# Kernel optimization log

Measured on AMD Instinct MI355X. Metric: run time of the kernel, lower is better.

## Reference

```python
import jax, jax.numpy as jnp
import numpy as np

VOCAB = 28996
EMBED = 512
N = 8192


def setup_inputs() -> dict:
    key = jax.random.key(0)
    k1, k2, k3, k4 = jax.random.split(key, 4)
    x = jax.random.normal(k1, (N, EMBED), dtype=jnp.float32)
    y = jax.random.randint(k2, (N,), 0, VOCAB, dtype=jnp.int64 if jax.config.jax_enable_x64 else jnp.int32)
    # nn.Linear params: weight (vocab, embed), bias (vocab,)
    W = jax.random.normal(k3, (VOCAB, EMBED), dtype=jnp.float32) * 0.02
    b = jax.random.normal(k4, (VOCAB,), dtype=jnp.float32) * 0.02
    return {"x": x, "y": y, "W": W, "b": b}


def reference(x, y, W, b):
    # Decoder: linear -> softmax over vocab (dim=1)
    logits = jnp.einsum("ne,ve->nv", x, W) + b          # (N, VOCAB)
    probs = jax.nn.softmax(logits, axis=1)              # first softmax (faithful to original)
    # nn.CrossEntropyLoss applied to probs: mean over nodes of
    #   logsumexp(probs) - probs[y]   (i.e., -log_softmax(probs)[y])
    logp = jax.nn.log_softmax(probs, axis=1)            # second (redundant) softmax pass
    nll = -jnp.take_along_axis(logp, y[:, None].astype(jnp.int32), axis=1)[:, 0]
    return jnp.mean(nll)
```

## Files before the change

### kernel.cpp

```cpp
#include <hip/hip_runtime.h>
#include <stdint.h>

#define VOCAB 28996
#define EMBED 512
#define NROWS 8192
#define VPAD  29056
#define LOG2E 1.4426950408889634f
#define WSCALE 16.0f
#define INV_WSCALE_L2E (LOG2E / 16.0f)

typedef __attribute__((ext_vector_type(4)))  int   i32x4;
typedef __attribute__((ext_vector_type(8)))  int   i32x8;
typedef __attribute__((ext_vector_type(16))) float f32x16;

__device__ __forceinline__ void gload_lds16(const void* g, void* l) {
  __builtin_amdgcn_global_load_lds(
      (__attribute__((address_space(1))) const void*)g,
      (__attribute__((address_space(3))) void*)l, 16, 0, 0);
}

__device__ __forceinline__ int pk_fp8x4(float a, float b, float c, float d) {
  int r = __builtin_amdgcn_cvt_pk_fp8_f32(a, b, 0, false);
  r = __builtin_amdgcn_cvt_pk_fp8_f32(c, d, r, true);
  return r;
}

__global__ void __launch_bounds__(256)
prep_kernel(const float* __restrict__ x, const float* __restrict__ W,
            const float* __restrict__ b, const int* __restrict__ y,
            int* __restrict__ xb, int* __restrict__ wb,
            float* __restrict__ py, float* __restrict__ sg) {
  const int bid = blockIdx.x;
  if (bid < 7264) {
    int i = (bid * 256 + threadIdx.x) * 8;
    const int VK = VOCAB * EMBED;
    int2 o;
    if (i < VK) {
      float4 v0 = *(const float4*)(W + i);
      float4 v1 = *(const float4*)(W + i + 4);
      o.x = pk_fp8x4(v0.x * WSCALE, v0.y * WSCALE, v0.z * WSCALE, v0.w * WSCALE);
      o.y = pk_fp8x4(v1.x * WSCALE, v1.y * WSCALE, v1.z * WSCALE, v1.w * WSCALE);
    } else { o.x = 0; o.y = 0; }
    *(int2*)(wb + i / 4) = o;
  } else if (bid < 9312) {
    int i = ((bid - 7264) * 256 + threadIdx.x) * 8;
    float4 v0 = *(const float4*)(x + i);
    float4 v1 = *(const float4*)(x + i + 4);
    int2 o;
    o.x = pk_fp8x4(v0.x, v0.y, v0.z, v0.w);
    o.y = pk_fp8x4(v1.x, v1.y, v1.z, v1.w);
    *(int2*)(xb + i / 4) = o;
  } else if (bid < 11360) {
    const int row  = ((bid - 9312) * 256 + threadIdx.x) >> 6;
    const int lane = threadIdx.x & 63;
    const int yr = y[row];
    const float4* xr = (const float4*)(x + (size_t)row * EMBED);
    const float4* wr = (const float4*)(W + (size_t)yr * EMBED);
    float d = 0.f;
#pragma unroll
    for (int t = 0; t < 2; ++t) {
      float4 a = xr[lane * 2 + t], c = wr[lane * 2 + t];
      d += a.x * c.x + a.y * c.y + a.z * c.z + a.w * c.w;
    }
#pragma unroll
    for (int m = 1; m < 64; m <<= 1) d += __shfl_xor(d, m);
    if (lane == 0) py[row] = __expf(d + b[yr]);
  } else {
    int i = (bid - 11360) * 256 + threadIdx.x;
    sg[i] = 0.f;
  }
}

__global__ void __launch_bounds__(512, 2)
gemm_stats_kernel(const uint8_t* __restrict__ xb, const uint8_t* __restrict__ wb,
                  const float* __restrict__ bias, float* __restrict__ sg) {
  __shared__ uint8_t lA[2][256 * 128];
  __shared__ uint8_t lB[2][256 * 128];

  const int tid  = threadIdx.x;
  const int lane = tid & 63;
  const int w    = tid >> 6;
  const int l31  = lane & 31;
  const int h    = lane >> 5;
  const int kx   = lane & 7;
  const int wr   = (w >> 2) * 128;
  const int wc   = (w & 3) * 64;
  const int rowBase = blockIdx.x * 256;
  const int colBase = blockIdx.y * 256;

  const int srow = lane >> 3;
  const int skel = (kx ^ srow) * 16;

  f32x16 acc[4][2];
#pragma unroll
  for (int i = 0; i < 4; ++i)
#pragma unroll
    for (int j = 0; j < 2; ++j)
#pragma unroll
      for (int r = 0; r < 16; ++r) acc[i][j][r] = 0.f;

  auto stage = [&](int buf, int k0) {
#pragma unroll
    for (int t = 0; t < 4; ++t) {
      const int c = w * 4 + t;
      const int ar = rowBase + c * 8;
      int br = colBase + c * 8;
      if (br > VPAD - 8) br = VPAD - 8;
      gload_lds16(xb + (size_t)(ar + srow) * EMBED + k0 + skel, &lA[buf][c * 1024]);
      gload_lds16(wb + (size_t)(br + srow) * EMBED + k0 + skel, &lB[buf][c * 1024]);
    }
  };

  stage(0, 0);

  const int aBase = (wr + l31) * 128;
  const int bBase = (wc + l31) * 128;

#pragma unroll
  for (int kt = 0; kt < 4; ++kt) {
    const int cur = kt & 1;
    __syncthreads();
    if (kt < 3) stage(cur ^ 1, (kt + 1) * 128);
    i32x8 bq[2][2];
#pragma unroll
    for (int kk = 0; kk < 2; ++kk) {
      const int c0 = ((kk * 4 + h * 2) ^ kx) << 4;
      const int c1 = c0 ^ 16;
#pragma unroll
      for (int ni = 0; ni < 2; ++ni) {
        const uint8_t* bp = &lB[cur][bBase + ni * 32 * 128];
        i32x4 lo = *(const i32x4*)(bp + c0);
        i32x4 hi = *(const i32x4*)(bp + c1);
        bq[kk][ni] = __builtin_shufflevector(lo, hi, 0, 1, 2, 3, 4, 5, 6, 7);
      }
    }
#pragma unroll
    for (int mi = 0; mi < 4; ++mi) {
      i32x8 af[2];
#pragma unroll
      for (int kk = 0; kk < 2; ++kk) {
        const int c0 = ((kk * 4 + h * 2) ^ kx) << 4;
        const int c1 = c0 ^ 16;
        const uint8_t* ap = &lA[cur][aBase + mi * 32 * 128];
        i32x4 lo = *(const i32x4*)(ap + c0);
        i32x4 hi = *(const i32x4*)(ap + c1);
        af[kk] = __builtin_shufflevector(lo, hi, 0, 1, 2, 3, 4, 5, 6, 7);
      }
      __builtin_amdgcn_s_setprio(1);
#pragma unroll
      for (int kk = 0; kk < 2; ++kk)
#pragma unroll
        for (int ni = 0; ni < 2; ++ni)
          acc[mi][ni] = __builtin_amdgcn_mfma_scale_f32_32x32x64_f8f6f4(
              af[kk], bq[kk][ni], acc[mi][ni], 0, 0, 0, 0x7F7F7F7F, 0, 0x7F7F7F7F);
      __builtin_amdgcn_s_setprio(0);
    }
  }

  float bvl[2];
#pragma unroll
  for (int ni = 0; ni < 2; ++ni) {
    const int col = colBase + wc + ni * 32 + l31;
    bvl[ni] = (col < VOCAB) ? bias[col] * LOG2E : -1e30f;
  }

#pragma unroll
  for (int p = 0; p < 2; ++p) {
    float sp[32];
#pragma unroll
    for (int q = 0; q < 2; ++q)
#pragma unroll
      for (int r = 0; r < 16; ++r)
        sp[q * 16 + r] =
            exp2f(fmaf(acc[p * 2 + q][0][r], INV_WSCALE_L2E, bvl[0])) +
            exp2f(fmaf(acc[p * 2 + q][1][r], INV_WSCALE_L2E, bvl[1]));

    float t1[16];
#pragma unroll
    for (int u = 0; u < 16; ++u) {
      float a = sp[2 * u]     + __shfl_xor(sp[2 * u],     1);
      float b = sp[2 * u + 1] + __shfl_xor(sp[2 * u + 1], 1);
      t1[u] = (l31 & 1) ? b : a;
    }
    float t2[8];
#pragma unroll
    for (int u = 0; u < 8; ++u) {
      float a = t1[2 * u]     + __shfl_xor(t1[2 * u],     2);
      float b = t1[2 * u + 1] + __shfl_xor(t1[2 * u + 1], 2);
      t2[u] = (l31 & 2) ? b : a;
    }
    float t3[4];
#pragma unroll
    for (int u = 0; u < 4; ++u) {
      float a = t2[2 * u]     + __shfl_xor(t2[2 * u],     4);
      float b = t2[2 * u + 1] + __shfl_xor(t2[2 * u + 1], 4);
      t3[u] = (l31 & 4) ? b : a;
    }
    float t4[2];
#pragma unroll
    for (int u = 0; u < 2; ++u) {
      float a = t3[2 * u]     + __shfl_xor(t3[2 * u],     8);
      float b = t3[2 * u + 1] + __shfl_xor(t3[2 * u + 1], 8);
      t4[u] = (l31 & 8) ? b : a;
    }
    {
      float a = t4[0] + __shfl_xor(t4[0], 16);
      float b = t4[1] + __shfl_xor(t4[1], 16);
      float ssum = (l31 & 16) ? b : a;
      const int v = l31;
      const int row = rowBase + wr + p * 64 + (v >> 4) * 32 +
                      (v & 3) + 8 * ((v & 15) >> 2) + 4 * h;
      atomicAdd(&sg[row], ssum);
    }
  }
}

__global__ void finalize_kernel(const float* __restrict__ sg, const float* __restrict__ py,
                                float* __restrict__ out) {
  __shared__ float red[256];
  float a = 0.f;
  for (int i = threadIdx.x; i < NROWS; i += 256)
    a += py[i] / sg[i];
  red[threadIdx.x] = a;
  __syncthreads();
  for (int st = 128; st > 0; st >>= 1) {
    if (threadIdx.x < st) red[threadIdx.x] += red[threadIdx.x + st];
    __syncthreads();
  }
  if (threadIdx.x == 0)
    out[0] = logf((float)(VOCAB + 1)) - red[0] * (1.f / (float)NROWS);
}

extern "C" void kernel_launch(void* const* d_in, const int* in_sizes, int n_in,
                              void* d_out, int out_size, void* d_ws, size_t ws_size,
                              hipStream_t stream) {
  const float* x = (const float*)d_in[0];
  const int*   y = (const int*)d_in[1];
  const float* W = (const float*)d_in[2];
  const float* b = (const float*)d_in[3];

  char* ws = (char*)d_ws;
  uint8_t* xb = (uint8_t*)ws;
  uint8_t* wb = (uint8_t*)(ws + 4194304);
  float*   sg = (float*)(ws + 4194304 + 14876672);
  float*   py = sg + NROWS;

  prep_kernel<<<11392, 256, 0, stream>>>(x, W, b, y, (int*)xb, (int*)wb, py, sg);
  gemm_stats_kernel<<<dim3(32, 114), 512, 0, stream>>>(xb, wb, b, sg);
  finalize_kernel<<<1, 256, 0, stream>>>(sg, py, (float*)d_out);
}
```

Before: 314.2 us.

## Interleave next-tile global-to-LDS loads with MFMA stages using explicit barriers

Restructures the K-loop of the FP8 GEMM so that prefetching of the next K tile is split across the mi iterations (A loads at mi=0, B loads at mi=1). The __syncthreads is replaced with explicit vmcnt/lgkmcnt waits, s_barrier and sched_barrier calls. The goal is to spread global memory issue between MFMA groups and keep waves in lockstep for better overlap. In exchange it adds more barriers per K step, which may cost sync overhead with only 4 K iterations.

```diff
diff --git a/kernel.cpp b/kernel.cpp
--- a/kernel.cpp
+++ b/kernel.cpp
@@ -99,19 +99,15 @@
 #pragma unroll
       for (int r = 0; r < 16; ++r) acc[i][j][r] = 0.f;
 
-  auto stage = [&](int buf, int k0) {
-#pragma unroll
-    for (int t = 0; t < 4; ++t) {
-      const int c = w * 4 + t;
-      const int ar = rowBase + c * 8;
-      int br = colBase + c * 8;
-      if (br > VPAD - 8) br = VPAD - 8;
-      gload_lds16(xb + (size_t)(ar + srow) * EMBED + k0 + skel, &lA[buf][c * 1024]);
-      gload_lds16(wb + (size_t)(br + srow) * EMBED + k0 + skel, &lB[buf][c * 1024]);
-    }
-  };
-
-  stage(0, 0);
+#pragma unroll
+  for (int t = 0; t < 4; ++t) {
+    const int c = w * 4 + t;
+    const int ar = rowBase + c * 8;
+    int br = colBase + c * 8;
+    if (br > VPAD - 8) br = VPAD - 8;
+    gload_lds16(xb + (size_t)(ar + srow) * EMBED + skel, &lA[0][c * 1024]);
+    gload_lds16(wb + (size_t)(br + srow) * EMBED + skel, &lB[0][c * 1024]);
+  }
 
   const int aBase = (wr + l31) * 128;
   const int bBase = (wc + l31) * 128;
@@ -119,33 +115,61 @@
 #pragma unroll
   for (int kt = 0; kt < 4; ++kt) {
     const int cur = kt & 1;
-    __syncthreads();
-    if (kt < 3) stage(cur ^ 1, (kt + 1) * 128);
+    asm volatile("s_waitcnt vmcnt(0)" ::: "memory");
+    __builtin_amdgcn_sched_barrier(0);
+    __builtin_amdgcn_s_barrier();
+
+    const uint8_t* __restrict__ Ab = lA[cur];
+    const uint8_t* __restrict__ Bb = lB[cur];
+    uint8_t* __restrict__ An = lA[cur ^ 1];
+    uint8_t* __restrict__ Bn = lB[cur ^ 1];
+    const int k1 = (kt + 1) * 128;
+
     i32x8 bq[2][2];
 #pragma unroll
-    for (int kk = 0; kk < 2; ++kk) {
-      const int c0 = ((kk * 4 + h * 2) ^ kx) << 4;
-      const int c1 = c0 ^ 16;
-#pragma unroll
-      for (int ni = 0; ni < 2; ++ni) {
-        const uint8_t* bp = &lB[cur][bBase + ni * 32 * 128];
-        i32x4 lo = *(const i32x4*)(bp + c0);
-        i32x4 hi = *(const i32x4*)(bp + c1);
-        bq[kk][ni] = __builtin_shufflevector(lo, hi, 0, 1, 2, 3, 4, 5, 6, 7);
+    for (int mi = 0; mi < 4; ++mi) {
+      if (mi == 0) {
+#pragma unroll
+        for (int kk = 0; kk < 2; ++kk) {
+          const int c0 = ((kk * 4 + h * 2) ^ kx) << 4;
+          const int c1 = c0 ^ 16;
+#pragma unroll
+          for (int ni = 0; ni < 2; ++ni) {
+            const uint8_t* bp = Bb + bBase + ni * 32 * 128;
+            i32x4 lo = *(const i32x4*)(bp + c0);
+            i32x4 hi = *(const i32x4*)(bp + c1);
+            bq[kk][ni] = __builtin_shufflevector(lo, hi, 0, 1, 2, 3, 4, 5, 6, 7);
+          }
+        }
       }
-    }
-#pragma unroll
-    for (int mi = 0; mi < 4; ++mi) {
       i32x8 af[2];
 #pragma unroll
       for (int kk = 0; kk < 2; ++kk) {
         const int c0 = ((kk * 4 + h * 2) ^ kx) << 4;
         const int c1 = c0 ^ 16;
-        const uint8_t* ap = &lA[cur][aBase + mi * 32 * 128];
+        const uint8_t* ap = Ab + aBase + mi * 32 * 128;
         i32x4 lo = *(const i32x4*)(ap + c0);
         i32x4 hi = *(const i32x4*)(ap + c1);
         af[kk] = __builtin_shufflevector(lo, hi, 0, 1, 2, 3, 4, 5, 6, 7);
       }
+      if (kt < 3 && mi < 2) {
+#pragma unroll
+        for (int t = 0; t < 4; ++t) {
+          const int c = w * 4 + t;
+          if (mi == 0) {
+            gload_lds16(xb + (size_t)(rowBase + c * 8 + srow) * EMBED + k1 + skel,
+                        An + c * 1024);
+          } else {
+            int br = colBase + c * 8;
+            if (br > VPAD - 8) br = VPAD - 8;
+            gload_lds16(wb + (size_t)(br + srow) * EMBED + k1 + skel,
+                        Bn + c * 1024);
+          }
+        }
+      }
+      __builtin_amdgcn_s_barrier();
+      asm volatile("s_waitcnt lgkmcnt(0)" ::: "memory");
+      __builtin_amdgcn_sched_barrier(0);
       __builtin_amdgcn_s_setprio(1);
 #pragma unroll
       for (int kk = 0; kk < 2; ++kk)
@@ -154,6 +178,7 @@
           acc[mi][ni] = __builtin_amdgcn_mfma_scale_f32_32x32x64_f8f6f4(
               af[kk], bq[kk][ni], acc[mi][ni], 0, 0, 0, 0x7F7F7F7F, 0, 0x7F7F7F7F);
       __builtin_amdgcn_s_setprio(0);
+      if (mi < 3) __builtin_amdgcn_s_barrier();
     }
   }
 
```

Result: slower. 324.7 us (+3.3%).

## Shrink GEMM tile to 128x256 with 256 threads and single-buffered LDS

Applied to the files above, without the earlier changes.

Changes the fused GEMM+softmax-stats kernel from 256x256 tiles with 8 waves and double-buffered LDS to 128x256 tiles with 4 waves and a single LDS buffer. Each k-step now loads, syncs, computes, and syncs again, with no prefetch overlap. The intent is to cut LDS use to 48KB per block so three blocks fit per CU, and to double the grid for better occupancy and load balance. In exchange it loses the software pipelining and the setprio hints, and each W tile is read twice as often.

```diff
diff --git a/kernel.cpp b/kernel.cpp
--- a/kernel.cpp
+++ b/kernel.cpp
@@ -71,11 +71,11 @@
   }
 }
 
-__global__ void __launch_bounds__(512, 2)
+__global__ void __launch_bounds__(256, 3)
 gemm_stats_kernel(const uint8_t* __restrict__ xb, const uint8_t* __restrict__ wb,
                   const float* __restrict__ bias, float* __restrict__ sg) {
-  __shared__ uint8_t lA[2][256 * 128];
-  __shared__ uint8_t lB[2][256 * 128];
+  __shared__ uint8_t lA[128 * 128];
+  __shared__ uint8_t lB[256 * 128];
 
   const int tid  = threadIdx.x;
   const int lane = tid & 63;
@@ -83,9 +83,8 @@
   const int l31  = lane & 31;
   const int h    = lane >> 5;
   const int kx   = lane & 7;
-  const int wr   = (w >> 2) * 128;
-  const int wc   = (w & 3) * 64;
-  const int rowBase = blockIdx.x * 256;
+  const int wc   = w * 64;
+  const int rowBase = blockIdx.x * 128;
   const int colBase = blockIdx.y * 256;
 
   const int srow = lane >> 3;
@@ -99,62 +98,55 @@
 #pragma unroll
       for (int r = 0; r < 16; ++r) acc[i][j][r] = 0.f;
 
-  auto stage = [&](int buf, int k0) {
+  auto stage = [&](int k0) {
 #pragma unroll
     for (int t = 0; t < 4; ++t) {
       const int c = w * 4 + t;
-      const int ar = rowBase + c * 8;
+      gload_lds16(xb + (size_t)(rowBase + c * 8 + srow) * EMBED + k0 + skel,
+                  &lA[c * 1024]);
+    }
+#pragma unroll
+    for (int t = 0; t < 8; ++t) {
+      const int c = w * 8 + t;
       int br = colBase + c * 8;
       if (br > VPAD - 8) br = VPAD - 8;
-      gload_lds16(xb + (size_t)(ar + srow) * EMBED + k0 + skel, &lA[buf][c * 1024]);
-      gload_lds16(wb + (size_t)(br + srow) * EMBED + k0 + skel, &lB[buf][c * 1024]);
+      gload_lds16(wb + (size_t)(br + srow) * EMBED + k0 + skel,
+                  &lB[c * 1024]);
     }
   };
 
-  stage(0, 0);
-
-  const int aBase = (wr + l31) * 128;
+  const int aBase = l31 * 128;
   const int bBase = (wc + l31) * 128;
 
 #pragma unroll
   for (int kt = 0; kt < 4; ++kt) {
-    const int cur = kt & 1;
+    stage(kt * 128);
     __syncthreads();
-    if (kt < 3) stage(cur ^ 1, (kt + 1) * 128);
-    i32x8 bq[2][2];
 #pragma unroll
     for (int kk = 0; kk < 2; ++kk) {
       const int c0 = ((kk * 4 + h * 2) ^ kx) << 4;
       const int c1 = c0 ^ 16;
+      i32x8 bq[2];
 #pragma unroll
       for (int ni = 0; ni < 2; ++ni) {
-        const uint8_t* bp = &lB[cur][bBase + ni * 32 * 128];
+        const uint8_t* bp = &lB[bBase + ni * 32 * 128];
         i32x4 lo = *(const i32x4*)(bp + c0);
         i32x4 hi = *(const i32x4*)(bp + c1);
-        bq[kk][ni] = __builtin_shufflevector(lo, hi, 0, 1, 2, 3, 4, 5, 6, 7);
+        bq[ni] = __builtin_shufflevector(lo, hi, 0, 1, 2, 3, 4, 5, 6, 7);
       }
-    }
-#pragma unroll
-    for (int mi = 0; mi < 4; ++mi) {
-      i32x8 af[2];
-#pragma unroll
-      for (int kk = 0; kk < 2; ++kk) {
-        const int c0 = ((kk * 4 + h * 2) ^ kx) << 4;
-        const int c1 = c0 ^ 16;
-        const uint8_t* ap = &lA[cur][aBase + mi * 32 * 128];
+#pragma unroll
+      for (int mi = 0; mi < 4; ++mi) {
+        const uint8_t* ap = &lA[aBase + mi * 32 * 128];
         i32x4 lo = *(const i32x4*)(ap + c0);
         i32x4 hi = *(const i32x4*)(ap + c1);
-        af[kk] = __builtin_shufflevector(lo, hi, 0, 1, 2, 3, 4, 5, 6, 7);
+        i32x8 af = __builtin_shufflevector(lo, hi, 0, 1, 2, 3, 4, 5, 6, 7);
+        acc[mi][0] = __builtin_amdgcn_mfma_scale_f32_32x32x64_f8f6f4(
+            af, bq[0], acc[mi][0], 0, 0, 0, 0x7F7F7F7F, 0, 0x7F7F7F7F);
+        acc[mi][1] = __builtin_amdgcn_mfma_scale_f32_32x32x64_f8f6f4(
+            af, bq[1], acc[mi][1], 0, 0, 0, 0x7F7F7F7F, 0, 0x7F7F7F7F);
       }
-      __builtin_amdgcn_s_setprio(1);
-#pragma unroll
-      for (int kk = 0; kk < 2; ++kk)
-#pragma unroll
-        for (int ni = 0; ni < 2; ++ni)
-          acc[mi][ni] = __builtin_amdgcn_mfma_scale_f32_32x32x64_f8f6f4(
-              af[kk], bq[kk][ni], acc[mi][ni], 0, 0, 0, 0x7F7F7F7F, 0, 0x7F7F7F7F);
-      __builtin_amdgcn_s_setprio(0);
-    }
+    }
+    __syncthreads();
   }
 
   float bvl[2];
@@ -208,7 +200,7 @@
       float b = t4[1] + __shfl_xor(t4[1], 16);
       float ssum = (l31 & 16) ? b : a;
       const int v = l31;
-      const int row = rowBase + wr + p * 64 + (v >> 4) * 32 +
+      const int row = rowBase + p * 64 + (v >> 4) * 32 +
                       (v & 3) + 8 * ((v & 15) >> 2) + 4 * h;
       atomicAdd(&sg[row], ssum);
     }
@@ -246,6 +238,6 @@
   float*   py = sg + NROWS;
 
   prep_kernel<<<11392, 256, 0, stream>>>(x, W, b, y, (int*)xb, (int*)wb, py, sg);
-  gemm_stats_kernel<<<dim3(32, 114), 512, 0, stream>>>(xb, wb, b, sg);
+  gemm_stats_kernel<<<dim3(64, 114), 256, 0, stream>>>(xb, wb, b, sg);
   finalize_kernel<<<1, 256, 0, stream>>>(sg, py, (float*)d_out);
 }
```

Result: slower. 791.4 us (+151.9%).
